# Kernel optimization log

Hardware: AMD Instinct MI355X
Metric: run time of the kernel (lower is better)

The kernel has to match this reference:

```python
import jax, jax.numpy as jnp
import numpy as np

B, S, D, H, DFF, L, R, V = 2, 1024, 1024, 16, 4096, 2, 3, 32000
HD = D // H


def layer_norm(x, g, b, eps=1e-5):
    mu = jnp.mean(x, axis=-1, keepdims=True)
    var = jnp.var(x, axis=-1, keepdims=True)
    return (x - mu) / jnp.sqrt(var + eps) * g + b


def recursion_block(x, mask, Wqkv, bqkv, Wo, bo, W1, b1, W2, b2, ln1_g, ln1_b, ln2_g, ln2_b):
    # shared pre-LN transformer stack of L layers, applied once per recursion step
    Bc, Sc, _ = x.shape
    scale = 1.0 / np.sqrt(HD).astype(np.float32)
    for l in range(L):
        h = layer_norm(x, ln1_g[l], ln1_b[l])
        qkv = h @ Wqkv[l] + bqkv[l]
        q, k, v = jnp.split(qkv, 3, axis=-1)
        q = q.reshape(Bc, Sc, H, HD).transpose(0, 2, 1, 3)
        k = k.reshape(Bc, Sc, H, HD).transpose(0, 2, 1, 3)
        v = v.reshape(Bc, Sc, H, HD).transpose(0, 2, 1, 3)
        scores = jnp.einsum('bhqd,bhkd->bhqk', q, k) * scale + mask
        attn = jax.nn.softmax(scores, axis=-1)
        o = jnp.einsum('bhqk,bhkd->bhqd', attn, v).transpose(0, 2, 1, 3).reshape(Bc, Sc, D)
        x = x + o @ Wo[l] + bo[l]
        h2 = layer_norm(x, ln2_g[l], ln2_b[l])
        x = x + jax.nn.gelu(h2 @ W1[l] + b1[l]) @ W2[l] + b2[l]
    return x


def setup_inputs() -> dict:
    key = jax.random.key(0)
    ks = jax.random.split(key, 12)
    n = lambda k, shape: (jax.random.normal(k, shape, jnp.float32) * 0.02)
    return {
        'input_ids': jax.random.randint(ks[0], (B, S), 0, V),
        'token_embed': n(ks[1], (V, D)),
        'pos_embed': n(ks[2], (S, D)),
        'Wqkv': n(ks[3], (L, D, 3 * D)), 'bqkv': jnp.zeros((L, 3 * D), jnp.float32),
        'Wo': n(ks[4], (L, D, D)), 'bo': jnp.zeros((L, D), jnp.float32),
        'W1': n(ks[5], (L, D, DFF)), 'b1': jnp.zeros((L, DFF), jnp.float32),
        'W2': n(ks[6], (L, DFF, D)), 'b2': jnp.zeros((L, D), jnp.float32),
        'ln1_g': jnp.ones((L, D), jnp.float32), 'ln1_b': jnp.zeros((L, D), jnp.float32),
        'ln2_g': jnp.ones((L, D), jnp.float32), 'ln2_b': jnp.zeros((L, D), jnp.float32),
        'final_g': jnp.ones((D,), jnp.float32), 'final_b': jnp.zeros((D,), jnp.float32),
        'Wr': n(ks[7], (D, R)), 'br': jnp.zeros((R,), jnp.float32),
    }


def reference(input_ids, token_embed, pos_embed, Wqkv, bqkv, Wo, bo, W1, b1, W2, b2,
              ln1_g, ln1_b, ln2_g, ln2_b, final_g, final_b, Wr, br):
    h = token_embed[input_ids] + pos_embed[None, :, :]            # [B,S,D]
    mask = jnp.where(jnp.tril(jnp.ones((S, S), bool)), 0.0, -jnp.inf)[None, None]  # [1,1,S,S]
    # token-choice router on detached hidden states
    rlogits = jax.lax.stop_gradient(h) @ Wr + br                  # [B,S,R]
    probs = jax.nn.softmax(rlogits, axis=-1)
    depth_map = jnp.argmax(rlogits, axis=-1) + 1                  # depths in 1..R
    importance = probs.mean(axis=(0, 1))
    router_loss = R * jnp.sum(importance ** 2)                    # load-balance aux loss
    res = h
    for step in range(R):
        step_mask = depth_map >= step + 1                         # [B,S] bool
        upd = recursion_block(res, mask, Wqkv, bqkv, Wo, bo, W1, b1, W2, b2,
                              ln1_g, ln1_b, ln2_g, ln2_b)
        res = jnp.where(step_mask[..., None], upd, res)
    hf = layer_norm(res, final_g, final_b)
    logits = hf @ token_embed.T                                   # tied lm_head
    return logits, depth_map, router_loss
```

## Files before the change

kernel.cpp:

```cpp
#include <hip/hip_runtime.h>
#include <hip/hip_bf16.h>

#define DD 1024
#define SS 1024
#define BB 2
#define HH 16
#define DFFN 4096
#define LLAYERS 2
#define RSTEPS 3
#define VV 32000
#define NTOK (BB*SS)

typedef __attribute__((ext_vector_type(8))) short s16x8;
typedef __attribute__((ext_vector_type(8))) __bf16 bf16x8;
typedef __attribute__((ext_vector_type(4))) float f32x4;

__device__ __forceinline__ unsigned short f2bf(float f) {
  unsigned int u = __float_as_uint(f);
  u += 0x7FFFu + ((u >> 16) & 1u);
  return (unsigned short)(u >> 16);
}

__device__ __forceinline__ f32x4 mfma16(s16x8 a, s16x8 b, f32x4 c) {
  return __builtin_amdgcn_mfma_f32_16x16x32_bf16(
      __builtin_bit_cast(bf16x8, a), __builtin_bit_cast(bf16x8, b), c, 0, 0, 0);
}

__device__ __forceinline__ void gload16(const unsigned short* g, unsigned short* l) {
  __builtin_amdgcn_global_load_lds(
      (const __attribute__((address_space(1))) unsigned int*)(const void*)g,
      (__attribute__((address_space(3))) unsigned int*)(void*)l, 16, 0, 0);
}

#define BAR()  asm volatile("s_barrier" ::: "memory")
#define LGK0() do { asm volatile("s_waitcnt lgkmcnt(0)" ::: "memory"); \
                    __builtin_amdgcn_sched_barrier(0); } while (0)
#define VM4()  asm volatile("s_waitcnt vmcnt(4)" ::: "memory")
#define VM0()  asm volatile("s_waitcnt vmcnt(0)" ::: "memory")

__global__ __launch_bounds__(256) void prep_all_kernel(
    const float* __restrict__ Wqkv, const float* __restrict__ Wo,
    const float* __restrict__ W1, const float* __restrict__ W2,
    const float* __restrict__ te,
    unsigned short* __restrict__ WqkvT, unsigned short* __restrict__ WoT,
    unsigned short* __restrict__ W1T, unsigned short* __restrict__ W2T,
    unsigned short* __restrict__ teb,
    const int* __restrict__ ids, const float* __restrict__ pe,
    const float* __restrict__ Wr, const float* __restrict__ br,
    float* __restrict__ res, float* __restrict__ probs,
    float* __restrict__ depth_ws, float* __restrict__ out_depth) {
  const int bid = blockIdx.x;
  const int tid = threadIdx.x;
  __shared__ unsigned short t[64][68];
  __shared__ float red[4][3];
  if (bid >= 22144) {
    int row = bid - 22144;
    int s = row & (SS - 1);
    int id = ids[row];
    int d = tid * 4;
    float4 a = *(const float4*)(te + (long)id * DD + d);
    float4 p = *(const float4*)(pe + (long)s * DD + d);
    float4 o; o.x = a.x + p.x; o.y = a.y + p.y; o.z = a.z + p.z; o.w = a.w + p.w;
    *(float4*)(res + (long)row * DD + d) = o;
    float a0 = 0.f, a1 = 0.f, a2 = 0.f;
    float hv[4] = {o.x, o.y, o.z, o.w};
#pragma unroll
    for (int j = 0; j < 4; ++j) {
      int dd = d + j;
      a0 += hv[j] * Wr[dd * 3 + 0];
      a1 += hv[j] * Wr[dd * 3 + 1];
      a2 += hv[j] * Wr[dd * 3 + 2];
    }
    for (int off = 32; off; off >>= 1) {
      a0 += __shfl_down(a0, off);
      a1 += __shfl_down(a1, off);
      a2 += __shfl_down(a2, off);
    }
    int wave = tid >> 6;
    if ((tid & 63) == 0) { red[wave][0] = a0; red[wave][1] = a1; red[wave][2] = a2; }
    __syncthreads();
    if (tid == 0) {
      a0 = red[0][0] + red[1][0] + red[2][0] + red[3][0] + br[0];
      a1 = red[0][1] + red[1][1] + red[2][1] + red[3][1] + br[1];
      a2 = red[0][2] + red[1][2] + red[2][2] + red[3][2] + br[2];
      float m = fmaxf(a0, fmaxf(a1, a2));
      float e0 = expf(a0 - m), e1 = expf(a1 - m), e2 = expf(a2 - m);
      float inv = 1.f / (e0 + e1 + e2);
      probs[row * 3 + 0] = e0 * inv;
      probs[row * 3 + 1] = e1 * inv;
      probs[row * 3 + 2] = e2 * inv;
      int am = 0; float bv = a0;
      if (a1 > bv) { bv = a1; am = 1; }
      if (a2 > bv) { bv = a2; am = 2; }
      float dm = (float)(am + 1);
      depth_ws[row] = dm;
      out_depth[row] = dm;
    }
    return;
  }
  if (bid >= 6144) {
    long i = ((long)(bid - 6144) * 256 + tid) * 8;
    float4 v0 = *(const float4*)(te + i);
    float4 v1 = *(const float4*)(te + i + 4);
    ushort4 a, b;
    a.x = f2bf(v0.x); a.y = f2bf(v0.y); a.z = f2bf(v0.z); a.w = f2bf(v0.w);
    b.x = f2bf(v1.x); b.y = f2bf(v1.y); b.z = f2bf(v1.z); b.w = f2bf(v1.w);
    *(ushort4*)(teb + i) = a;
    *(ushort4*)(teb + i + 4) = b;
    return;
  }
  const float* src; unsigned short* dst; int Kd, Nd, local;
  if (bid < 1536) {
    int l = (bid >= 768);
    local = bid - l * 768;
    src = Wqkv + (long)l * DD * 3 * DD; dst = WqkvT + (long)l * 3 * DD * DD;
    Kd = DD; Nd = 3 * DD;
  } else if (bid < 2048) {
    int l = (bid - 1536) >> 8; local = (bid - 1536) & 255;
    src = Wo + (long)l * DD * DD; dst = WoT + (long)l * DD * DD;
    Kd = DD; Nd = DD;
  } else if (bid < 4096) {
    int l = (bid - 2048) >> 10; local = (bid - 2048) & 1023;
    src = W1 + (long)l * DD * DFFN; dst = W1T + (long)l * DFFN * DD;
    Kd = DD; Nd = DFFN;
  } else {
    int l = (bid - 4096) >> 10; local = (bid - 4096) & 1023;
    src = W2 + (long)l * DFFN * DD; dst = W2T + (long)l * DD * DFFN;
    Kd = DFFN; Nd = DD;
  }
  const int tn = Nd >> 6;
  const int n0 = (local % tn) * 64, k0 = (local / tn) * 64;
#pragma unroll
  for (int c = 0; c < 4; ++c) {
    int p = tid + c * 256;
    int kr = p >> 4, nc = (p & 15) * 4;
    float4 v = *(const float4*)(src + (long)(k0 + kr) * Nd + n0 + nc);
    t[nc + 0][kr] = f2bf(v.x);
    t[nc + 1][kr] = f2bf(v.y);
    t[nc + 2][kr] = f2bf(v.z);
    t[nc + 3][kr] = f2bf(v.w);
  }
  __syncthreads();
#pragma unroll
  for (int c = 0; c < 4; ++c) {
    int p = tid + c * 256;
    int nr = p >> 4, kc = (p & 15) * 4;
    ushort4 o;
    o.x = t[nr][kc]; o.y = t[nr][kc + 1]; o.z = t[nr][kc + 2]; o.w = t[nr][kc + 3];
    *(ushort4*)(dst + (long)(n0 + nr) * Kd + k0 + kc) = o;
  }
}

__global__ __launch_bounds__(256) void router_finalize_kernel(
    const float* __restrict__ probs, float* __restrict__ out_loss) {
  __shared__ float red[256][3];
  int t = threadIdx.x;
  float s0 = 0.f, s1 = 0.f, s2 = 0.f;
  for (int r = t; r < NTOK; r += 256) {
    s0 += probs[r * 3 + 0]; s1 += probs[r * 3 + 1]; s2 += probs[r * 3 + 2];
  }
  red[t][0] = s0; red[t][1] = s1; red[t][2] = s2;
  __syncthreads();
  for (int off = 128; off; off >>= 1) {
    if (t < off) {
      red[t][0] += red[t + off][0];
      red[t][1] += red[t + off][1];
      red[t][2] += red[t + off][2];
    }
    __syncthreads();
  }
  if (t == 0) {
    float i0 = red[0][0] / NTOK, i1 = red[0][1] / NTOK, i2 = red[0][2] / NTOK;
    out_loss[0] = (float)RSTEPS * (i0 * i0 + i1 * i1 + i2 * i2);
  }
}

__global__ __launch_bounds__(256) void ln_kernel(
    const float* __restrict__ x, const float* __restrict__ g,
    const float* __restrict__ b, unsigned short* __restrict__ y) {
  int row = blockIdx.x;
  int t = threadIdx.x;
  float4 v = *(const float4*)(x + (long)row * DD + t * 4);
  float s = v.x + v.y + v.z + v.w;
  float q = v.x * v.x + v.y * v.y + v.z * v.z + v.w * v.w;
  for (int off = 32; off; off >>= 1) {
    s += __shfl_down(s, off);
    q += __shfl_down(q, off);
  }
  __shared__ float rs[4], rq[4];
  int wave = t >> 6;
  if ((t & 63) == 0) { rs[wave] = s; rq[wave] = q; }
  __syncthreads();
  float S_ = rs[0] + rs[1] + rs[2] + rs[3];
  float Q_ = rq[0] + rq[1] + rq[2] + rq[3];
  float mu = S_ * (1.f / DD);
  float var = Q_ * (1.f / DD) - mu * mu;
  float rstd = rsqrtf(var + 1e-5f);
  int d = t * 4;
  float4 gg = *(const float4*)(g + d);
  float4 bb = *(const float4*)(b + d);
  ushort4 ov;
  ov.x = f2bf((v.x - mu) * rstd * gg.x + bb.x);
  ov.y = f2bf((v.y - mu) * rstd * gg.y + bb.y);
  ov.z = f2bf((v.z - mu) * rstd * gg.z + bb.z);
  ov.w = f2bf((v.w - mu) * rstd * gg.w + bb.w);
  *(ushort4*)(y + (long)row * DD + d) = ov;
}

__device__ __forceinline__ void stageA8(unsigned short* S, int buf, int qm,
    const unsigned short* A, int lda, long m0, int kt, int tid) {
  unsigned short* dst = S + buf * 32768 + qm * 8192;
#pragma unroll
  for (int c = 0; c < 2; ++c) {
    int idx = tid + c * 512;
    int L = (idx << 4) ^ (((idx >> 5) & 1) << 5);
    int band = L >> 13, row = (L >> 7) & 63, kel = (L & 127) >> 1;
    gload16(A + (m0 + band * 128 + qm * 64 + row) * (long)lda + kt * 64 + kel,
            dst + idx * 8);
  }
}

__device__ __forceinline__ void stageB8(unsigned short* S, int buf, int qn,
    const unsigned short* Bt, int ldb, long n0, int kt, int tid) {
  unsigned short* dst = S + buf * 32768 + 16384 + qn * 8192;
#pragma unroll
  for (int c = 0; c < 2; ++c) {
    int idx = tid + c * 512;
    int L = (idx << 4) ^ (((idx >> 5) & 1) << 5);
    int band = L >> 12, row = (L >> 7) & 31, kel = (L & 127) >> 1;
    gload16(Bt + (n0 + band * 64 + qn * 32 + row) * (long)ldb + kt * 64 + kel,
            dst + idx * 8);
  }
}

__device__ __forceinline__ void read_af8(const unsigned short* S, int base,
    int wm, int l16, int g, s16x8 af[2][4]) {
  const int swz = ((l16 >> 2) & 1) << 5;
#pragma unroll
  for (int kk = 0; kk < 2; ++kk)
#pragma unroll
    for (int mf = 0; mf < 4; ++mf) {
      int L = (wm * 8192 + (mf * 16 + l16) * 128 + (kk * 32 + g * 8) * 2) ^ swz;
      af[kk][mf] = *(const s16x8*)(S + base + (L >> 1));
    }
}

__device__ __forceinline__ void read_bf8(const unsigned short* S, int base,
    int wn, int l16, int g, s16x8 bf[2][2]) {
  const int swz = ((l16 >> 2) & 1) << 5;
#pragma unroll
  for (int kk = 0; kk < 2; ++kk)
#pragma unroll
    for (int nf = 0; nf < 2; ++nf) {
      int L = (wn * 4096 + (nf * 16 + l16) * 128 + (kk * 32 + g * 8) * 2) ^ swz;
      bf[kk][nf] = *(const s16x8*)(S + base + (L >> 1));
    }
}

template<int QM, int QN>
__device__ __forceinline__ void do_mfma8(f32x4 acc[8][4],
    const s16x8 af[2][4], const s16x8 bf[2][2]) {
  __builtin_amdgcn_s_setprio(1);
#pragma unroll
  for (int kk = 0; kk < 2; ++kk)
#pragma unroll
    for (int mf = 0; mf < 4; ++mf)
#pragma unroll
      for (int nf = 0; nf < 2; ++nf)
        acc[QM * 4 + mf][QN * 2 + nf] =
            mfma16(af[kk][mf], bf[kk][nf], acc[QM * 4 + mf][QN * 2 + nf]);
  __builtin_amdgcn_s_setprio(0);
}

template<int CBF16, int BIAS, int GELU_ACT>
__global__ __launch_bounds__(512, 1) void gemm256_kernel(
    const unsigned short* __restrict__ A, int lda,
    const unsigned short* __restrict__ Bt, int ldb,
    void* __restrict__ Cv, int ldc,
    const float* __restrict__ bias, int K, int Mblocks) {
  __shared__ unsigned short S[65536];
  const int tid = threadIdx.x;
  const int lane = tid & 63, wave = tid >> 6;
  const int g = lane >> 4, l16 = lane & 15;
  const int wm = wave >> 2, wn = wave & 3;
  const int nwg = gridDim.x * gridDim.y;
  const int orig = blockIdx.x + blockIdx.y * gridDim.x;
  const int q = nwg >> 3, r = nwg & 7;
  const int xcd = orig & 7, loc = orig >> 3;
  const int wgid = (xcd < r ? xcd * (q + 1) : r * (q + 1) + (xcd - r) * q) + loc;
  const long m0 = (long)(wgid % Mblocks) * 256;
  const long n0 = (long)(wgid / Mblocks) * 256;

  f32x4 acc[8][4] = {};
  s16x8 af[2][4], bf[2][2];
  const int NI = K >> 7;

  stageA8(S, 0, 0, A, lda, m0, 0, tid);
  stageA8(S, 0, 1, A, lda, m0, 0, tid);
  stageB8(S, 0, 0, Bt, ldb, n0, 0, tid);
  stageB8(S, 0, 1, Bt, ldb, n0, 0, tid);
  stageA8(S, 1, 0, A, lda, m0, 1, tid);
  stageB8(S, 1, 1, Bt, ldb, n0, 1, tid);
  VM4(); BAR();

  for (int i = 0; i < NI; ++i) {
    const int kt1 = 2 * i + 1, kt2 = 2 * i + 2, kt3 = 2 * i + 3;
    const bool more = (i + 1 < NI);
    read_af8(S, 0, wm, l16, g, af);
    read_bf8(S, 16384, wn, l16, g, bf);
    stageA8(S, 1, 1, A, lda, m0, kt1, tid);
    BAR(); LGK0();
    do_mfma8<0, 0>(acc, af, bf);
    BAR();
    read_bf8(S, 16384 + 8192, wn, l16, g, bf);
    stageB8(S, 1, 0, Bt, ldb, n0, kt1, tid);
    BAR(); LGK0();
    do_mfma8<0, 1>(acc, af, bf);
    BAR();
    read_af8(S, 8192, wm, l16, g, af);
    if (more) stageA8(S, 0, 0, A, lda, m0, kt2, tid);
    BAR(); LGK0();
    do_mfma8<1, 1>(acc, af, bf);
    BAR();
    read_bf8(S, 16384, wn, l16, g, bf);
    if (more) stageB8(S, 0, 1, Bt, ldb, n0, kt2, tid);
    BAR(); LGK0();
    do_mfma8<1, 0>(acc, af, bf);
    if (more) { VM4(); } else { VM0(); }
    BAR();
    read_af8(S, 32768, wm, l16, g, af);
    read_bf8(S, 32768 + 16384, wn, l16, g, bf);
    if (more) stageA8(S, 0, 1, A, lda, m0, kt2, tid);
    BAR(); LGK0();
    do_mfma8<0, 0>(acc, af, bf);
    BAR();
    read_bf8(S, 32768 + 16384 + 8192, wn, l16, g, bf);
    if (more) stageB8(S, 0, 0, Bt, ldb, n0, kt2, tid);
    BAR(); LGK0();
    do_mfma8<0, 1>(acc, af, bf);
    BAR();
    read_af8(S, 32768 + 8192, wm, l16, g, af);
    if (more) stageA8(S, 1, 0, A, lda, m0, kt3, tid);
    BAR(); LGK0();
    do_mfma8<1, 1>(acc, af, bf);
    BAR();
    read_bf8(S, 32768 + 16384, wn, l16, g, bf);
    if (more) stageB8(S, 1, 1, Bt, ldb, n0, kt3, tid);
    BAR(); LGK0();
    do_mfma8<1, 0>(acc, af, bf);
    VM4(); BAR();
  }

#pragma unroll
  for (int mf = 0; mf < 8; ++mf) {
#pragma unroll
    for (int nf = 0; nf < 4; ++nf) {
      long row0 = m0 + wm * 128 + mf * 16 + g * 4;
      long col = n0 + wn * 64 + nf * 16 + l16;
      float bv = BIAS ? bias[col] : 0.f;
#pragma unroll
      for (int rr = 0; rr < 4; ++rr) {
        float v = acc[mf][nf][rr] + bv;
        if (GELU_ACT) {
          float x3 = v * v * v;
          v = 0.5f * v * (1.f + tanhf(0.7978845608028654f * (v + 0.044715f * x3)));
        }
        if (CBF16) ((unsigned short*)Cv)[(row0 + rr) * (long)ldc + col] = f2bf(v);
        else       ((float*)Cv)[(row0 + rr) * (long)ldc + col] = v;
      }
    }
  }
}

template<int BN, int CBF16, int BIAS, int RESID, int GELU_ACT, int QKVW>
__global__ __launch_bounds__(256) void gemm128_kernel(
    const unsigned short* __restrict__ A, int lda,
    const unsigned short* __restrict__ Bt, int ldb,
    void* __restrict__ Cv, int ldc,
    const float* __restrict__ bias,
    const float* __restrict__ resid, int ldr,
    unsigned short* __restrict__ vtw,
    int K) {
  constexpr int BM = 128;
  constexpr int WN = BN / 2;
  constexpr int MR = 4;
  constexpr int NR = WN / 16;
  __shared__ unsigned short As[BM * 64];
  __shared__ unsigned short Bs[BN * 64];
  const int tid = threadIdx.x;
  const int lane = tid & 63, wave = tid >> 6;
  const int g = lane >> 4, l16 = lane & 15;
  const int wr = wave >> 1, wc = wave & 1;
  int lin = blockIdx.x + blockIdx.y * gridDim.x;
  int per = (gridDim.x * gridDim.y) >> 3;
  int v = (lin & 7) * per + (lin >> 3);
  const long m0 = (long)(v % gridDim.y) * BM;
  const long n0 = (long)(v / gridDim.y) * BN;
  f32x4 acc[MR][NR] = {};
  for (int k0 = 0; k0 < K; k0 += 64) {
    __syncthreads();
#pragma unroll
    for (int c = 0; c < BM / 32; ++c) {
      int p = tid + c * 256;
      int r = p >> 3, kq = (p & 7) * 8;
      gload16(A + (m0 + r) * (long)lda + k0 + kq, &As[p * 8]);
    }
#pragma unroll
    for (int c = 0; c < BN / 32; ++c) {
      int p = tid + c * 256;
      int r = p >> 3, kq = (p & 7) * 8;
      gload16(Bt + (n0 + r) * (long)ldb + k0 + kq, &Bs[p * 8]);
    }
    __syncthreads();
#pragma unroll
    for (int kk = 0; kk < 2; ++kk) {
      s16x8 af[MR], bf[NR];
#pragma unroll
      for (int m = 0; m < MR; ++m)
        af[m] = *(const s16x8*)&As[(wr * 64 + m * 16 + l16) * 64 + kk * 32 + g * 8];
#pragma unroll
      for (int n = 0; n < NR; ++n)
        bf[n] = *(const s16x8*)&Bs[(wc * WN + n * 16 + l16) * 64 + kk * 32 + g * 8];
#pragma unroll
      for (int m = 0; m < MR; ++m)
#pragma unroll
        for (int n = 0; n < NR; ++n)
          acc[m][n] = mfma16(af[m], bf[n], acc[m][n]);
    }
  }
  const bool vblk = QKVW && (n0 >= 2048);
#pragma unroll
  for (int m = 0; m < MR; ++m) {
#pragma unroll
    for (int n = 0; n < NR; ++n) {
      long row_base = m0 + wr * 64 + m * 16 + g * 4;
      long col = n0 + wc * WN + n * 16 + l16;
      float bv = BIAS ? bias[col] : 0.f;
      float vv4[4];
#pragma unroll
      for (int r = 0; r < 4; ++r) {
        long row = row_base + r;
        float vv = acc[m][n][r] + bv;
        if (RESID) vv += resid[row * (long)ldr + col];
        if (GELU_ACT) {
          float x3 = vv * vv * vv;
          vv = 0.5f * vv * (1.f + tanhf(0.7978845608028654f * (vv + 0.044715f * x3)));
        }
        vv4[r] = vv;
      }
      if (QKVW && vblk) {
        int rel = (int)col - 2048;
        int h = rel >> 6, d = rel & 63;
        int b = (int)(row_base >> 10);
        int s = (int)(row_base & 1023);
        ushort4 o;
        o.x = f2bf(vv4[0]); o.y = f2bf(vv4[1]);
        o.z = f2bf(vv4[2]); o.w = f2bf(vv4[3]);
        *(ushort4*)(vtw + (((long)(b * 16 + h) * 64 + d) * SS + s)) = o;
      } else {
#pragma unroll
        for (int r = 0; r < 4; ++r) {
          long row = row_base + r;
          if (CBF16) ((unsigned short*)Cv)[row * (long)ldc + col] = f2bf(vv4[r]);
          else       ((float*)Cv)[row * (long)ldc + col] = vv4[r];
        }
      }
    }
  }
}

template<int CBF16, int BIAS, int RESID, int SELW>
__global__ __launch_bounds__(512) void gemm64w8_kernel(
    const unsigned short* __restrict__ A, int lda,
    const unsigned short* __restrict__ Bt, int ldb,
    void* __restrict__ Cv, int ldc,
    const float* __restrict__ bias,
    const float* __restrict__ resid, int ldr,
    const float* __restrict__ depth_ws, float stepf,
    int K) {
  __shared__ unsigned short As[128 * 64];
  __shared__ unsigned short Bs[64 * 64];
  const int tid = threadIdx.x;
  const int lane = tid & 63, wave = tid >> 6;
  const int g = lane >> 4, l16 = lane & 15;
  const int wr = wave >> 1, wc = wave & 1;
  int lin = blockIdx.x + blockIdx.y * gridDim.x;
  int per = (gridDim.x * gridDim.y) >> 3;
  int v = (lin & 7) * per + (lin >> 3);
  const long m0 = (long)(v % gridDim.y) * 128;
  const long n0 = (long)(v / gridDim.y) * 64;
  f32x4 acc[2][2] = {};
  for (int k0 = 0; k0 < K; k0 += 64) {
    __syncthreads();
#pragma unroll
    for (int c = 0; c < 2; ++c) {
      int p = tid + c * 512;
      int r = p >> 3, kq = (p & 7) * 8;
      gload16(A + (m0 + r) * (long)lda + k0 + kq, &As[p * 8]);
    }
    {
      int r = tid >> 3, kq = (tid & 7) * 8;
      gload16(Bt + (n0 + r) * (long)ldb + k0 + kq, &Bs[tid * 8]);
    }
    __syncthreads();
#pragma unroll
    for (int kk = 0; kk < 2; ++kk) {
      s16x8 af[2], bf[2];
#pragma unroll
      for (int m = 0; m < 2; ++m)
        af[m] = *(const s16x8*)&As[(wr * 32 + m * 16 + l16) * 64 + kk * 32 + g * 8];
#pragma unroll
      for (int n = 0; n < 2; ++n)
        bf[n] = *(const s16x8*)&Bs[(wc * 32 + n * 16 + l16) * 64 + kk * 32 + g * 8];
#pragma unroll
      for (int m = 0; m < 2; ++m)
#pragma unroll
        for (int n = 0; n < 2; ++n)
          acc[m][n] = mfma16(af[m], bf[n], acc[m][n]);
    }
  }
#pragma unroll
  for (int m = 0; m < 2; ++m) {
#pragma unroll
    for (int n = 0; n < 2; ++n) {
      long row_base = m0 + wr * 32 + m * 16 + g * 4;
      long col = n0 + wc * 32 + n * 16 + l16;
      float bv = BIAS ? bias[col] : 0.f;
#pragma unroll
      for (int r = 0; r < 4; ++r) {
        long row = row_base + r;
        float vv = acc[m][n][r] + bv;
        if (RESID) vv += resid[row * (long)ldr + col];
        if (SELW) {
          if (depth_ws[row] >= stepf)
            ((float*)Cv)[row * (long)ldc + col] = vv;
        } else if (CBF16) {
          ((unsigned short*)Cv)[row * (long)ldc + col] = f2bf(vv);
        } else {
          ((float*)Cv)[row * (long)ldc + col] = vv;
        }
      }
    }
  }
}

__global__ __launch_bounds__(256) void attn_kernel(
    const unsigned short* __restrict__ qkv,
    const unsigned short* __restrict__ vt,
    unsigned short* __restrict__ o) {
  __shared__ unsigned short Ks[2][64 * 64];
  __shared__ unsigned short Vs[2][64 * 64];
  __shared__ unsigned short Pl[4][16][72];
  const int qb = gridDim.x - 1 - blockIdx.x;
  const int bh = blockIdx.y;
  const int b = bh >> 4, h = bh & 15;
  const int tid = threadIdx.x, wave = tid >> 6, lane = tid & 63;
  const int g = lane >> 4, l16 = lane & 15;
  const float NEG_INF = -__builtin_inff();
  const int q0 = qb * 64;
  const int qrw = q0 + wave * 16;
  const long rowbase = (long)b * SS;
  const unsigned short* kbase = qkv + rowbase * 3072 + 1024 + h * 64;
  const unsigned short* vbase = vt + (long)bh * 64 * SS;

  const unsigned short* qptr = qkv + (rowbase + qrw + l16) * 3072 + h * 64;
  s16x8 qf0 = *(const s16x8*)(qptr + g * 8);
  s16x8 qf1 = *(const s16x8*)(qptr + 32 + g * 8);

  f32x4 oacc[4] = {};
  float mrun = NEG_INF, lrun = 0.f;

  const int ntile = q0 / 64 + 1;

#pragma unroll
  for (int c = 0; c < 2; ++c) {
    int idx = tid + c * 256;
    int r = idx >> 3;
    int bo = (idx & 7) * 16;
    int sw = (bo ^ ((r & 7) << 4)) >> 1;
    gload16(kbase + (long)r * 3072 + sw, &Ks[0][idx * 8]);
    gload16(vbase + (long)r * SS + 0 + sw, &Vs[0][idx * 8]);
  }
  asm volatile("s_waitcnt vmcnt(0)" ::: "memory");
  __syncthreads();

  for (int t = 0; t < ntile; ++t) {
    const int cur = t & 1;
    const int kv0 = t * 64;
    const unsigned short* ks_cur = &Ks[cur][0];
    const unsigned short* vs_cur = &Vs[cur][0];
    if (t + 1 < ntile) {
      const int kvn = kv0 + 64;
#pragma unroll
      for (int c = 0; c < 2; ++c) {
        int idx = tid + c * 256;
        int r = idx >> 3;
        int bo = (idx & 7) * 16;
        int sw = (bo ^ ((r & 7) << 4)) >> 1;
        gload16(kbase + (long)(kvn + r) * 3072 + sw, &Ks[cur ^ 1][idx * 8]);
        gload16(vbase + (long)r * SS + kvn + sw, &Vs[cur ^ 1][idx * 8]);
      }
    }
    f32x4 accs[4] = {};
#pragma unroll
    for (int ks = 0; ks < 2; ++ks) {
#pragma unroll
      for (int kvb = 0; kvb < 4; ++kvb) {
        int row = kvb * 16 + l16;
        int bo = ((ks * 64 + g * 16) ^ ((l16 & 7) << 4)) >> 1;
        s16x8 kf = *(const s16x8*)&ks_cur[row * 64 + bo];
        accs[kvb] = mfma16(kf, ks ? qf1 : qf0, accs[kvb]);
      }
    }
    const bool needmask = (kv0 + 63 > qrw);
    const int qabs = qrw + l16;
    float sv[4][4];
    float mloc = NEG_INF;
#pragma unroll
    for (int kvb = 0; kvb < 4; ++kvb) {
#pragma unroll
      for (int r = 0; r < 4; ++r) {
        float vv = accs[kvb][r] * 0.125f;
        if (needmask) {
          int kva = kv0 + kvb * 16 + g * 4 + r;
          if (kva > qabs) vv = NEG_INF;
        }
        sv[kvb][r] = vv;
        mloc = fmaxf(mloc, vv);
      }
    }
    mloc = fmaxf(mloc, __shfl_xor(mloc, 16));
    mloc = fmaxf(mloc, __shfl_xor(mloc, 32));
    float mnew = fmaxf(mrun, mloc);
    float alpha = __expf(mrun - mnew);
    float lsum = 0.f;
#pragma unroll
    for (int kvb = 0; kvb < 4; ++kvb) {
      float p0 = __expf(sv[kvb][0] - mnew);
      float p1 = __expf(sv[kvb][1] - mnew);
      float p2 = __expf(sv[kvb][2] - mnew);
      float p3 = __expf(sv[kvb][3] - mnew);
      lsum += (p0 + p1) + (p2 + p3);
      unsigned int w0 = (unsigned)f2bf(p0) | ((unsigned)f2bf(p1) << 16);
      unsigned int w1 = (unsigned)f2bf(p2) | ((unsigned)f2bf(p3) << 16);
      uint2 pw; pw.x = w0; pw.y = w1;
      *(uint2*)&Pl[wave][l16][kvb * 16 + g * 4] = pw;
    }
    lsum += __shfl_xor(lsum, 16);
    lsum += __shfl_xor(lsum, 32);
    lrun = lrun * alpha + lsum;
    mrun = mnew;
    float mult[4];
#pragma unroll
    for (int r = 0; r < 4; ++r) mult[r] = __shfl(alpha, g * 4 + r);
#pragma unroll
    for (int nd = 0; nd < 4; ++nd)
#pragma unroll
      for (int r = 0; r < 4; ++r) oacc[nd][r] *= mult[r];
#pragma unroll
    for (int kh = 0; kh < 2; ++kh) {
      s16x8 pa = *(const s16x8*)&Pl[wave][l16][kh * 32 + g * 8];
#pragma unroll
      for (int nd = 0; nd < 4; ++nd) {
        int row = nd * 16 + l16;
        int bo = ((kh * 64 + g * 16) ^ ((l16 & 7) << 4)) >> 1;
        s16x8 vf = *(const s16x8*)&vs_cur[row * 64 + bo];
        oacc[nd] = mfma16(pa, vf, oacc[nd]);
      }
    }
    asm volatile("s_waitcnt vmcnt(0)" ::: "memory");
    __syncthreads();
  }
  unsigned short* ob = o + (rowbase + qrw) * 1024 + h * 64;
#pragma unroll
  for (int r = 0; r < 4; ++r) {
    float lr = __shfl(lrun, g * 4 + r);
    float inv = 1.f / lr;
#pragma unroll
    for (int nd = 0; nd < 4; ++nd)
      ob[(long)(g * 4 + r) * 1024 + nd * 16 + l16] = f2bf(oacc[nd][r] * inv);
  }
}

extern "C" void kernel_launch(void* const* d_in, const int* in_sizes, int n_in,
                              void* d_out, int out_size, void* d_ws, size_t ws_size,
                              hipStream_t stream) {
  (void)in_sizes; (void)n_in; (void)out_size; (void)ws_size;
  const int*   ids  = (const int*)d_in[0];
  const float* te   = (const float*)d_in[1];
  const float* pe   = (const float*)d_in[2];
  const float* Wqkv = (const float*)d_in[3];
  const float* bqkv = (const float*)d_in[4];
  const float* Wo   = (const float*)d_in[5];
  const float* bo   = (const float*)d_in[6];
  const float* W1   = (const float*)d_in[7];
  const float* b1   = (const float*)d_in[8];
  const float* W2   = (const float*)d_in[9];
  const float* b2   = (const float*)d_in[10];
  const float* ln1g = (const float*)d_in[11];
  const float* ln1b = (const float*)d_in[12];
  const float* ln2g = (const float*)d_in[13];
  const float* ln2b = (const float*)d_in[14];
  const float* fing = (const float*)d_in[15];
  const float* finb = (const float*)d_in[16];
  const float* Wr   = (const float*)d_in[17];
  const float* br   = (const float*)d_in[18];

  float* logits    = (float*)d_out;
  float* out_depth = logits + (long)NTOK * VV;
  float* out_loss  = out_depth + NTOK;

  char* w = (char*)d_ws;
  float* res            = (float*)w;          w += (long)NTOK * DD * 4;
  float* x              = (float*)w;          w += (long)NTOK * DD * 4;
  unsigned short* hbuf  = (unsigned short*)w; w += (long)NTOK * DD * 2;
  unsigned short* qkvb  = (unsigned short*)w; w += (long)NTOK * 3 * DD * 2;
  unsigned short* obuf  = (unsigned short*)w; w += (long)NTOK * DD * 2;
  unsigned short* ffn1  = (unsigned short*)w; w += (long)NTOK * DFFN * 2;
  unsigned short* vtb   = (unsigned short*)w; w += (long)BB * HH * 64 * SS * 2;
  float* probs          = (float*)w;          w += (long)NTOK * 3 * 4;
  float* depth_ws       = (float*)w;          w += (long)NTOK * 4;
  unsigned short* WqkvT = (unsigned short*)w; w += (long)LLAYERS * 3 * DD * DD * 2;
  unsigned short* WoT   = (unsigned short*)w; w += (long)LLAYERS * DD * DD * 2;
  unsigned short* W1T   = (unsigned short*)w; w += (long)LLAYERS * DFFN * DD * 2;
  unsigned short* W2T   = (unsigned short*)w; w += (long)LLAYERS * DD * DFFN * 2;
  unsigned short* teb   = (unsigned short*)w; w += (long)VV * DD * 2;

  prep_all_kernel<<<6144 + 16000 + NTOK, 256, 0, stream>>>(
      Wqkv, Wo, W1, W2, te, WqkvT, WoT, W1T, W2T, teb,
      ids, pe, Wr, br, res, probs, depth_ws, out_depth);
  router_finalize_kernel<<<1, 256, 0, stream>>>(probs, out_loss);

  for (int step = 0; step < RSTEPS; ++step) {
    for (int l = 0; l < LLAYERS; ++l) {
      const float* xin = (l == 0) ? res : x;
      ln_kernel<<<NTOK, 256, 0, stream>>>(xin, ln1g + l * DD, ln1b + l * DD, hbuf);
      gemm128_kernel<128, 1, 1, 0, 0, 1><<<dim3(3 * DD / 128, NTOK / 128), 256, 0, stream>>>(
          hbuf, DD, WqkvT + (long)l * 3 * DD * DD, DD, qkvb, 3 * DD,
          bqkv + (long)l * 3 * DD, nullptr, 0, vtb, DD);
      attn_kernel<<<dim3(SS / 64, BB * HH), 256, 0, stream>>>(qkvb, vtb, obuf);
      gemm64w8_kernel<0, 1, 1, 0><<<dim3(DD / 64, NTOK / 128), 512, 0, stream>>>(
          obuf, DD, WoT + (long)l * DD * DD, DD, x, DD,
          bo + (long)l * DD, xin, DD, nullptr, 0.f, DD);
      ln_kernel<<<NTOK, 256, 0, stream>>>(x, ln2g + l * DD, ln2b + l * DD, hbuf);
      gemm128_kernel<128, 1, 1, 0, 1, 0><<<dim3(DFFN / 128, NTOK / 128), 256, 0, stream>>>(
          hbuf, DD, W1T + (long)l * DFFN * DD, DD, ffn1, DFFN,
          b1 + (long)l * DFFN, nullptr, 0, nullptr, DD);
      if (l == 0) {
        gemm64w8_kernel<0, 1, 1, 0><<<dim3(DD / 64, NTOK / 128), 512, 0, stream>>>(
            ffn1, DFFN, W2T + (long)l * DD * DFFN, DFFN, x, DD,
            b2 + (long)l * DD, x, DD, nullptr, 0.f, DFFN);
      } else {
        gemm64w8_kernel<0, 1, 1, 1><<<dim3(DD / 64, NTOK / 128), 512, 0, stream>>>(
            ffn1, DFFN, W2T + (long)l * DD * DFFN, DFFN, res, DD,
            b2 + (long)l * DD, x, DD, depth_ws, (float)(step + 1), DFFN);
      }
    }
  }
  ln_kernel<<<NTOK, 256, 0, stream>>>(res, fing, finb, hbuf);
  gemm256_kernel<0, 0, 0><<<dim3(VV / 256, NTOK / 256), 512, 0, stream>>>(
      hbuf, DD, teb, DD, logits, VV, nullptr, DD, NTOK / 256);
}
```

Before: 1.464 ms.

## Double-buffer GEMM LDS tiles and widen attention blocks to 128 queries

Both GEMM kernels now keep two LDS buffers and prefetch the next K tile with global_load_lds while the current tile is computed, using vmcnt waits and raw barriers in place of two __syncthreads per iteration. The attention kernel moves to 512 threads covering 128 query rows per block, so each K/V tile is loaded once and shared by twice as many waves, with one load per thread per tile. The aim is to hide global-load latency and cut redundant K/V traffic. The cost is doubled LDS use in the GEMMs, which may lower occupancy, and fewer, larger attention blocks with a coarser causal tiling.

```diff
diff --git a/kernel.cpp b/kernel.cpp
--- a/kernel.cpp
+++ b/kernel.cpp
@@ -35,7 +35,9 @@
 #define BAR()  asm volatile("s_barrier" ::: "memory")
 #define LGK0() do { asm volatile("s_waitcnt lgkmcnt(0)" ::: "memory"); \
                     __builtin_amdgcn_sched_barrier(0); } while (0)
+#define VM8()  asm volatile("s_waitcnt vmcnt(8)" ::: "memory")
 #define VM4()  asm volatile("s_waitcnt vmcnt(4)" ::: "memory")
+#define VM3()  asm volatile("s_waitcnt vmcnt(3)" ::: "memory")
 #define VM0()  asm volatile("s_waitcnt vmcnt(0)" ::: "memory")
 
 __global__ __launch_bounds__(256) void prep_all_kernel(
@@ -385,8 +387,9 @@
   constexpr int WN = BN / 2;
   constexpr int MR = 4;
   constexpr int NR = WN / 16;
-  __shared__ unsigned short As[BM * 64];
-  __shared__ unsigned short Bs[BN * 64];
+  static_assert(BM / 32 + BN / 32 == 8, "vmcnt(8) literal assumes 8 loads/thread");
+  __shared__ unsigned short As[2][BM * 64];
+  __shared__ unsigned short Bs[2][BN * 64];
   const int tid = threadIdx.x;
   const int lane = tid & 63, wave = tid >> 6;
   const int g = lane >> 4, l16 = lane & 15;
@@ -397,36 +400,46 @@
   const long m0 = (long)(v % gridDim.y) * BM;
   const long n0 = (long)(v / gridDim.y) * BN;
   f32x4 acc[MR][NR] = {};
-  for (int k0 = 0; k0 < K; k0 += 64) {
-    __syncthreads();
+  const int NT = K >> 6;
+
+  auto stage = [&](int buf, int kt) {
+    const int k0 = kt * 64;
 #pragma unroll
     for (int c = 0; c < BM / 32; ++c) {
       int p = tid + c * 256;
       int r = p >> 3, kq = (p & 7) * 8;
-      gload16(A + (m0 + r) * (long)lda + k0 + kq, &As[p * 8]);
+      gload16(A + (m0 + r) * (long)lda + k0 + kq, &As[buf][p * 8]);
     }
 #pragma unroll
     for (int c = 0; c < BN / 32; ++c) {
       int p = tid + c * 256;
       int r = p >> 3, kq = (p & 7) * 8;
-      gload16(Bt + (n0 + r) * (long)ldb + k0 + kq, &Bs[p * 8]);
-    }
-    __syncthreads();
+      gload16(Bt + (n0 + r) * (long)ldb + k0 + kq, &Bs[buf][p * 8]);
+    }
+  };
+
+  stage(0, 0);
+  for (int kt = 0; kt < NT; ++kt) {
+    const int cur = kt & 1;
+    const bool more = (kt + 1 < NT);
+    if (more) { stage(cur ^ 1, kt + 1); VM8(); } else { VM0(); }
+    BAR();
 #pragma unroll
     for (int kk = 0; kk < 2; ++kk) {
       s16x8 af[MR], bf[NR];
 #pragma unroll
       for (int m = 0; m < MR; ++m)
-        af[m] = *(const s16x8*)&As[(wr * 64 + m * 16 + l16) * 64 + kk * 32 + g * 8];
+        af[m] = *(const s16x8*)&As[cur][(wr * 64 + m * 16 + l16) * 64 + kk * 32 + g * 8];
 #pragma unroll
       for (int n = 0; n < NR; ++n)
-        bf[n] = *(const s16x8*)&Bs[(wc * WN + n * 16 + l16) * 64 + kk * 32 + g * 8];
+        bf[n] = *(const s16x8*)&Bs[cur][(wc * WN + n * 16 + l16) * 64 + kk * 32 + g * 8];
 #pragma unroll
       for (int m = 0; m < MR; ++m)
 #pragma unroll
         for (int n = 0; n < NR; ++n)
           acc[m][n] = mfma16(af[m], bf[n], acc[m][n]);
     }
+    BAR();
   }
   const bool vblk = QKVW && (n0 >= 2048);
 #pragma unroll
@@ -478,8 +491,8 @@
     const float* __restrict__ resid, int ldr,
     const float* __restrict__ depth_ws, float stepf,
     int K) {
-  __shared__ unsigned short As[128 * 64];
-  __shared__ unsigned short Bs[64 * 64];
+  __shared__ unsigned short As[2][128 * 64];
+  __shared__ unsigned short Bs[2][64 * 64];
   const int tid = threadIdx.x;
   const int lane = tid & 63, wave = tid >> 6;
   const int g = lane >> 4, l16 = lane & 15;
@@ -490,34 +503,44 @@
   const long m0 = (long)(v % gridDim.y) * 128;
   const long n0 = (long)(v / gridDim.y) * 64;
   f32x4 acc[2][2] = {};
-  for (int k0 = 0; k0 < K; k0 += 64) {
-    __syncthreads();
+  const int NT = K >> 6;
+
+  auto stage = [&](int buf, int kt) {
+    const int k0 = kt * 64;
 #pragma unroll
     for (int c = 0; c < 2; ++c) {
       int p = tid + c * 512;
       int r = p >> 3, kq = (p & 7) * 8;
-      gload16(A + (m0 + r) * (long)lda + k0 + kq, &As[p * 8]);
+      gload16(A + (m0 + r) * (long)lda + k0 + kq, &As[buf][p * 8]);
     }
     {
       int r = tid >> 3, kq = (tid & 7) * 8;
-      gload16(Bt + (n0 + r) * (long)ldb + k0 + kq, &Bs[tid * 8]);
-    }
-    __syncthreads();
+      gload16(Bt + (n0 + r) * (long)ldb + k0 + kq, &Bs[buf][tid * 8]);
+    }
+  };
+
+  stage(0, 0);
+  for (int kt = 0; kt < NT; ++kt) {
+    const int cur = kt & 1;
+    const bool more = (kt + 1 < NT);
+    if (more) { stage(cur ^ 1, kt + 1); VM3(); } else { VM0(); }
+    BAR();
 #pragma unroll
     for (int kk = 0; kk < 2; ++kk) {
       s16x8 af[2], bf[2];
 #pragma unroll
       for (int m = 0; m < 2; ++m)
-        af[m] = *(const s16x8*)&As[(wr * 32 + m * 16 + l16) * 64 + kk * 32 + g * 8];
+        af[m] = *(const s16x8*)&As[cur][(wr * 32 + m * 16 + l16) * 64 + kk * 32 + g * 8];
 #pragma unroll
       for (int n = 0; n < 2; ++n)
-        bf[n] = *(const s16x8*)&Bs[(wc * 32 + n * 16 + l16) * 64 + kk * 32 + g * 8];
+        bf[n] = *(const s16x8*)&Bs[cur][(wc * 32 + n * 16 + l16) * 64 + kk * 32 + g * 8];
 #pragma unroll
       for (int m = 0; m < 2; ++m)
 #pragma unroll
         for (int n = 0; n < 2; ++n)
           acc[m][n] = mfma16(af[m], bf[n], acc[m][n]);
     }
+    BAR();
   }
 #pragma unroll
   for (int m = 0; m < 2; ++m) {
@@ -544,20 +567,20 @@
   }
 }
 
-__global__ __launch_bounds__(256) void attn_kernel(
+__global__ __launch_bounds__(512) void attn_kernel(
     const unsigned short* __restrict__ qkv,
     const unsigned short* __restrict__ vt,
     unsigned short* __restrict__ o) {
   __shared__ unsigned short Ks[2][64 * 64];
   __shared__ unsigned short Vs[2][64 * 64];
-  __shared__ unsigned short Pl[4][16][72];
+  __shared__ unsigned short Pl[8][16][72];
   const int qb = gridDim.x - 1 - blockIdx.x;
   const int bh = blockIdx.y;
   const int b = bh >> 4, h = bh & 15;
   const int tid = threadIdx.x, wave = tid >> 6, lane = tid & 63;
   const int g = lane >> 4, l16 = lane & 15;
   const float NEG_INF = -__builtin_inff();
-  const int q0 = qb * 64;
+  const int q0 = qb * 128;
   const int qrw = q0 + wave * 16;
   const long rowbase = (long)b * SS;
   const unsigned short* kbase = qkv + rowbase * 3072 + 1024 + h * 64;
@@ -570,16 +593,14 @@
   f32x4 oacc[4] = {};
   float mrun = NEG_INF, lrun = 0.f;
 
-  const int ntile = q0 / 64 + 1;
-
-#pragma unroll
-  for (int c = 0; c < 2; ++c) {
-    int idx = tid + c * 256;
-    int r = idx >> 3;
-    int bo = (idx & 7) * 16;
+  const int ntile = q0 / 64 + 2;
+
+  {
+    int r = tid >> 3;
+    int bo = (tid & 7) * 16;
     int sw = (bo ^ ((r & 7) << 4)) >> 1;
-    gload16(kbase + (long)r * 3072 + sw, &Ks[0][idx * 8]);
-    gload16(vbase + (long)r * SS + 0 + sw, &Vs[0][idx * 8]);
+    gload16(kbase + (long)r * 3072 + sw, &Ks[0][tid * 8]);
+    gload16(vbase + (long)r * SS + 0 + sw, &Vs[0][tid * 8]);
   }
   asm volatile("s_waitcnt vmcnt(0)" ::: "memory");
   __syncthreads();
@@ -591,15 +612,11 @@
     const unsigned short* vs_cur = &Vs[cur][0];
     if (t + 1 < ntile) {
       const int kvn = kv0 + 64;
-#pragma unroll
-      for (int c = 0; c < 2; ++c) {
-        int idx = tid + c * 256;
-        int r = idx >> 3;
-        int bo = (idx & 7) * 16;
-        int sw = (bo ^ ((r & 7) << 4)) >> 1;
-        gload16(kbase + (long)(kvn + r) * 3072 + sw, &Ks[cur ^ 1][idx * 8]);
-        gload16(vbase + (long)r * SS + kvn + sw, &Vs[cur ^ 1][idx * 8]);
-      }
+      int r = tid >> 3;
+      int bo = (tid & 7) * 16;
+      int sw = (bo ^ ((r & 7) << 4)) >> 1;
+      gload16(kbase + (long)(kvn + r) * 3072 + sw, &Ks[cur ^ 1][tid * 8]);
+      gload16(vbase + (long)r * SS + kvn + sw, &Vs[cur ^ 1][tid * 8]);
     }
     f32x4 accs[4] = {};
 #pragma unroll
@@ -738,7 +755,7 @@
       gemm128_kernel<128, 1, 1, 0, 0, 1><<<dim3(3 * DD / 128, NTOK / 128), 256, 0, stream>>>(
           hbuf, DD, WqkvT + (long)l * 3 * DD * DD, DD, qkvb, 3 * DD,
           bqkv + (long)l * 3 * DD, nullptr, 0, vtb, DD);
-      attn_kernel<<<dim3(SS / 64, BB * HH), 256, 0, stream>>>(qkvb, vtb, obuf);
+      attn_kernel<<<dim3(SS / 128, BB * HH), 512, 0, stream>>>(qkvb, vtb, obuf);
       gemm64w8_kernel<0, 1, 1, 0><<<dim3(DD / 64, NTOK / 128), 512, 0, stream>>>(
           obuf, DD, WoT + (long)l * DD * DD, DD, x, DD,
           bo + (long)l * DD, xin, DD, nullptr, 0.f, DD);
```

After: 1.363 ms. 1.07x faster.
